# Kernel optimization log

Measured on AMD Instinct MI355X. Metric: run time of the kernel, lower is better.

## Reference

```python
import jax, jax.numpy as jnp
import numpy as np

EMBED = 768
HEADS = 12
HEAD_DIM = EMBED // HEADS
B, S = 1, 4096


def setup_inputs() -> dict:
    key = jax.random.key(0)
    ks = jax.random.split(key, 8)
    values = jax.random.normal(ks[0], (B, S, EMBED), dtype=jnp.float32)
    keys_in = jax.random.normal(ks[1], (B, S, EMBED), dtype=jnp.float32)
    queries = jax.random.normal(ks[2], (B, S, EMBED), dtype=jnp.float32)
    # causal mask: 1.0 where attention is disallowed (gets * -1e9)
    mask = jnp.triu(jnp.ones((S, S), dtype=jnp.float32), k=1)[None, None, :, :]
    sc = 1.0 / np.sqrt(EMBED)
    W_q = jax.random.normal(ks[3], (EMBED, EMBED), dtype=jnp.float32) * sc
    W_k = jax.random.normal(ks[4], (EMBED, EMBED), dtype=jnp.float32) * sc
    W_v = jax.random.normal(ks[5], (EMBED, EMBED), dtype=jnp.float32) * sc
    W_o = jax.random.normal(ks[6], (EMBED, EMBED), dtype=jnp.float32) * sc
    b_o = jnp.zeros((EMBED,), dtype=jnp.float32)
    return {"values": values, "keys": keys_in, "queries": queries, "mask": mask,
            "W_q": W_q, "W_k": W_k, "W_v": W_v, "W_o": W_o, "b_o": b_o}


def reference(values, keys, queries, mask, W_q, W_k, W_v, W_o, b_o):
    N, S_, _ = queries.shape
    # linear projections (Dense, no bias)
    q = queries @ W_q  # [N, S, E]
    k = keys @ W_k
    v = values @ W_v
    # split heads -> [N, H, S, Dh]
    def split(x):
        return x.reshape(N, S_, HEADS, HEAD_DIM).transpose(0, 2, 1, 3)
    q, k, v = split(q), split(k), split(v)
    scores = jnp.einsum('nhqd,nhkd->nhqk', q, k) / jnp.sqrt(
        jnp.asarray(HEAD_DIM, dtype=q.dtype))
    scores = scores + mask * (-1e9)
    attn = jax.nn.softmax(scores, axis=-1)
    out = jnp.einsum('nhqk,nhkd->nhqd', attn, v)  # [N, H, S, Dh]
    out = out.transpose(0, 2, 1, 3).reshape(N, S_, EMBED)
    return out @ W_o + b_o
```

## Files before the change

### kernel.cpp

```cpp
#include <hip/hip_runtime.h>

#define S_LEN 4096
#define EMB   768
#define NH    12
#define DH    64

typedef __attribute__((ext_vector_type(8))) short bf16x8;
typedef __attribute__((ext_vector_type(4))) float f32x4;

__device__ __forceinline__ unsigned short f2bf(float f) {
    union { float f; unsigned u; } v; v.f = f;
    unsigned r = v.u + 0x7fffu + ((v.u >> 16) & 1u);
    return (unsigned short)(r >> 16);
}
__device__ __forceinline__ float bf2f(unsigned short u) {
    union { unsigned u; float f; } v; v.u = (unsigned)u << 16; return v.f;
}
__device__ __forceinline__ unsigned pk2(float lo, float hi) {
    unsigned r;
    asm("v_cvt_pk_bf16_f32 %0, %1, %2" : "=v"(r) : "v"(lo), "v"(hi));
    return r;
}
__device__ __forceinline__ float fexp2(float x) {
    float r;
    asm("v_exp_f32 %0, %1" : "=v"(r) : "v"(x));
    return r;
}
__device__ __forceinline__ f32x4 mfma16(bf16x8 a, bf16x8 b, f32x4 c) {
    return __builtin_amdgcn_mfma_f32_16x16x32_bf16(a, b, c, 0, 0, 0);
}
__device__ __forceinline__ void async16(unsigned short* lds, const unsigned short* g) {
    __builtin_amdgcn_global_load_lds(
        (const __attribute__((address_space(1))) unsigned int*)(const void*)g,
        (__attribute__((address_space(3))) unsigned int*)(void*)lds, 16, 0, 0);
}

#define QSCALE 0.180336884f

__global__ __launch_bounds__(256) void prep(const float* __restrict__ Wq, const float* __restrict__ Wk,
                     const float* __restrict__ Wv, const float* __restrict__ Wo,
                     const float* __restrict__ q_in, const float* __restrict__ k_in,
                     const float* __restrict__ v_in,
                     unsigned short* __restrict__ WT, unsigned short* __restrict__ conv) {
    int bx = blockIdx.x, t = threadIdx.x;
    if (bx < 576) {
        __shared__ float tile[64][65];
        int z = bx / 144, rem = bx % 144;
        int k0 = (rem / 12) * 64, n0 = (rem % 12) * 64;
        const float* W = (z == 0) ? Wq : (z == 1) ? Wk : (z == 2) ? Wv : Wo;
        unsigned short* out = WT + (size_t)z * EMB * EMB;
        int row = t >> 2, c = (t & 3) * 16;
        const float4* src = (const float4*)(W + (size_t)(k0 + row) * EMB + n0 + c);
#pragma unroll
        for (int i = 0; i < 4; i++) {
            float4 v = src[i];
            tile[row][c + i * 4 + 0] = v.x; tile[row][c + i * 4 + 1] = v.y;
            tile[row][c + i * 4 + 2] = v.z; tile[row][c + i * 4 + 3] = v.w;
        }
        __syncthreads();
        unsigned short tmp[16] __attribute__((aligned(16)));
#pragma unroll
        for (int i = 0; i < 16; i++) tmp[i] = f2bf(tile[c + i][row]);
        int4* dst = (int4*)(out + (size_t)(n0 + row) * EMB + k0 + c);
        dst[0] = *(int4*)&tmp[0];
        dst[1] = *(int4*)&tmp[8];
    } else {
        size_t e8 = ((size_t)(bx - 576) * 256 + t) * 8;
        int z = (int)(e8 / 3145728);
        size_t off = e8 - (size_t)z * 3145728;
        const float* src = (z == 0) ? q_in : (z == 1) ? k_in : v_in;
        float4 a = *(const float4*)(src + off);
        float4 b = *(const float4*)(src + off + 4);
        unsigned r[4];
        r[0] = pk2(a.x, a.y); r[1] = pk2(a.z, a.w);
        r[2] = pk2(b.x, b.y); r[3] = pk2(b.z, b.w);
        *(int4*)(conv + e8) = *(int4*)r;
    }
}


__global__ __launch_bounds__(256) void gemm_qkv(const unsigned short* __restrict__ conv,
                                                const unsigned short* __restrict__ WT,
                                                unsigned short* __restrict__ Qh,
                                                unsigned short* __restrict__ Kh,
                                                unsigned short* __restrict__ Vt) {
    __shared__ unsigned short As[128 * 32];
    __shared__ unsigned short Bs[128 * 32];
    int m0 = blockIdx.x * 128;
    int z = blockIdx.y / 6, n0 = (blockIdx.y % 6) * 128;
    const unsigned short* A  = conv + (size_t)z * 3145728;
    const unsigned short* Bt = WT   + (size_t)z * 589824;
    int t = threadIdx.x, lane = t & 63, wv = t >> 6, quad = lane >> 4, l16 = lane & 15;
    int wm = wv >> 1, wn = wv & 1;
    int cfr = (quad ^ ((l16 >> 1) & 3)) * 8;

    const unsigned short* pa[2];
    const unsigned short* pb[2];
#pragma unroll
    for (int a2 = 0; a2 < 2; a2++) {
        int s1 = a2 * 256 + t, r = s1 >> 2, gc = (s1 & 3) ^ ((r >> 1) & 3);
        pa[a2] = A  + (size_t)(m0 + r) * EMB + gc * 8;
        pb[a2] = Bt + (size_t)(n0 + r) * EMB + gc * 8;
    }
    f32x4 acc[4][4] = {};

    for (int k0 = 0; k0 < EMB; k0 += 32) {
#pragma unroll
        for (int a2 = 0; a2 < 2; a2++) {
            async16(&As[(a2 * 256 + t) * 8], pa[a2] + k0);
            async16(&Bs[(a2 * 256 + t) * 8], pb[a2] + k0);
        }
        __syncthreads();
        bf16x8 fa[4], fb[4];
#pragma unroll
        for (int mi = 0; mi < 4; mi++)
            fa[mi] = *(bf16x8*)&As[(wm * 64 + mi * 16 + l16) * 32 + cfr];
#pragma unroll
        for (int ni = 0; ni < 4; ni++)
            fb[ni] = *(bf16x8*)&Bs[(wn * 64 + ni * 16 + l16) * 32 + cfr];
#pragma unroll
        for (int mi = 0; mi < 4; mi++)
#pragma unroll
            for (int ni = 0; ni < 4; ni++)
                acc[mi][ni] = mfma16(fa[mi], fb[ni], acc[mi][ni]);
        __syncthreads();
    }

    if (z == 2) {
#pragma unroll
        for (int mi = 0; mi < 4; mi++)
#pragma unroll
            for (int ni = 0; ni < 4; ni++) {
                int m = m0 + wm * 64 + mi * 16 + quad * 4;
                int n = n0 + wn * 64 + ni * 16 + l16;
                uint2 val;
                val.x = pk2(acc[mi][ni][0], acc[mi][ni][1]);
                val.y = pk2(acc[mi][ni][2], acc[mi][ni][3]);
                *(uint2*)&Vt[(size_t)(((n >> 6) << 6) + (n & 63)) * S_LEN + m] = val;
            }
    } else {
        unsigned short* dst = z ? Kh : Qh;
        float sc = z ? 1.0f : QSCALE;
#pragma unroll
        for (int mi = 0; mi < 4; mi++)
#pragma unroll
            for (int ni = 0; ni < 4; ni++)
#pragma unroll
                for (int r = 0; r < 4; r++) {
                    int m = m0 + wm * 64 + mi * 16 + quad * 4 + r;
                    int n = n0 + wn * 64 + ni * 16 + l16;
                    dst[((size_t)(n >> 6) * S_LEN + m) * 64 + (n & 63)] = f2bf(acc[mi][ni][r] * sc);
                }
    }
}

__global__ __launch_bounds__(256) void attn_kernel(const unsigned short* __restrict__ Qh,
                                                   const unsigned short* __restrict__ Kh,
                                                   const unsigned short* __restrict__ Vt,
                                                   unsigned short* __restrict__ Opart,
                                                   float* __restrict__ Lpart) {
    __shared__ unsigned short Kls[2][4096];
    __shared__ unsigned short Vls[2][4096];
    __shared__ unsigned short Pls[4 * 64 * 72];

    int p = blockIdx.x, h = blockIdx.y;
    int qb = 0, pre = 0, np = 1;
    for (;;) { np = (4 * qb + 9) / 6; if (pre + np > p) break; pre += np; qb++; }
    int sp = p - pre;
    int ntile = 4 * qb + 4;
    int base = ntile / np, rem = ntile % np;
    int jb = sp * base + min(sp, rem);
    int je = jb + base + (sp < rem ? 1 : 0);
    int part = h * 96 + p;
    int q0 = qb << 8;

    int t = threadIdx.x, w = t >> 6, lane = t & 63, quad = lane >> 4, l16 = lane & 15;
    int rb = w * 64;
    int cfr0 = (quad ^ (l16 & 7)) * 8, cfr1 = ((quad + 4) ^ (l16 & 7)) * 8;

    const unsigned short* kb_ = Kh + (size_t)h * S_LEN * DH;
    const unsigned short* vb_ = Vt + (size_t)h * S_LEN * DH;

    bf16x8 aQ[4][2];
#pragma unroll
    for (int rg = 0; rg < 4; rg++)
#pragma unroll
        for (int kh = 0; kh < 2; kh++)
            aQ[rg][kh] = *(const bf16x8*)(Qh + ((size_t)h * S_LEN + q0 + rb + rg * 16 + l16) * 64 + kh * 32 + quad * 8);

    const unsigned short* pk_[2];
    const unsigned short* pv_[2];
#pragma unroll
    for (int a2 = 0; a2 < 2; a2++) {
        int s1 = a2 * 256 + t, r = s1 >> 3, gc = (s1 & 7) ^ (r & 7);
        pk_[a2] = kb_ + (size_t)(jb * 64 + r) * 64 + gc * 8;
        pv_[a2] = vb_ + (size_t)r * S_LEN + jb * 64 + gc * 8;
    }

    f32x4 o[4][4] = {};
    float lsum[4][4] = {};
    unsigned short* pwave = &Pls[w * 64 * 72];

    for (int jt = jb; jt < je; jt++) {
        int buf = (jt - jb) & 1;
        if (jt == jb) {
#pragma unroll
            for (int a2 = 0; a2 < 2; a2++) {
                async16(&Kls[0][(a2 * 256 + t) * 8], pk_[a2]); pk_[a2] += 4096;
                async16(&Vls[0][(a2 * 256 + t) * 8], pv_[a2]); pv_[a2] += 64;
            }
        }
        __syncthreads();
        if (jt + 1 < je) {
#pragma unroll
            for (int a2 = 0; a2 < 2; a2++) {
                async16(&Kls[buf ^ 1][(a2 * 256 + t) * 8], pk_[a2]); pk_[a2] += 4096;
                async16(&Vls[buf ^ 1][(a2 * 256 + t) * 8], pv_[a2]); pv_[a2] += 64;
            }
        }
        int diag = jt - 4 * qb;
        bool active = !(diag >= 0 && w < diag);
        if (active) {
            bf16x8 kf[4][2];
#pragma unroll
            for (int nt = 0; nt < 4; nt++) {
                int row = nt * 16 + l16;
                kf[nt][0] = *(bf16x8*)&Kls[buf][row * 64 + cfr0];
                kf[nt][1] = *(bf16x8*)&Kls[buf][row * 64 + cfr1];
            }
#pragma unroll
            for (int rg = 0; rg < 4; rg++) {
                f32x4 s[4];
#pragma unroll
                for (int nt = 0; nt < 4; nt++) {
                    f32x4 zz = {};
                    zz = mfma16(aQ[rg][0], kf[nt][0], zz);
                    zz = mfma16(aQ[rg][1], kf[nt][1], zz);
                    s[nt] = zz;
                }
                if (diag >= 0) {
                    int dlt = diag * 64;
#pragma unroll
                    for (int nt = 0; nt < 4; nt++) {
                        int col = nt * 16 + l16;
#pragma unroll
                        for (int r = 0; r < 4; r++) {
                            int rel = rb + rg * 16 + quad * 4 + r - dlt;
                            if (col > rel) s[nt][r] = -1e9f;
                        }
                    }
                }
#pragma unroll
                for (int nt = 0; nt < 4; nt++) {
                    float p0 = fexp2(s[nt][0]);
                    float p1 = fexp2(s[nt][1]);
                    float p2 = fexp2(s[nt][2]);
                    float p3 = fexp2(s[nt][3]);
                    lsum[rg][0] += p0; lsum[rg][1] += p1;
                    lsum[rg][2] += p2; lsum[rg][3] += p3;
                    unsigned pa2 = pk2(p0, p1), pb2 = pk2(p2, p3);
                    unsigned short* pw = &pwave[(rg * 16 + quad * 4) * 72 + nt * 16 + l16];
                    pw[0]   = (unsigned short)pa2;
                    pw[72]  = (unsigned short)(pa2 >> 16);
                    pw[144] = (unsigned short)pb2;
                    pw[216] = (unsigned short)(pb2 >> 16);
                }
            }
            asm volatile("s_waitcnt lgkmcnt(0)" ::: "memory");
            bf16x8 bP[4][2];
#pragma unroll
            for (int ntq = 0; ntq < 4; ntq++) {
                bP[ntq][0] = *(bf16x8*)&pwave[(ntq * 16 + l16) * 72 + quad * 8];
                bP[ntq][1] = *(bf16x8*)&pwave[(ntq * 16 + l16) * 72 + 32 + quad * 8];
            }
#pragma unroll
            for (int mt = 0; mt < 4; mt++) {
                int row = mt * 16 + l16;
                bf16x8 v0f = *(bf16x8*)&Vls[buf][row * 64 + cfr0];
                bf16x8 v1f = *(bf16x8*)&Vls[buf][row * 64 + cfr1];
#pragma unroll
                for (int ntq = 0; ntq < 4; ntq++) {
                    o[mt][ntq] = mfma16(v0f, bP[ntq][0], o[mt][ntq]);
                    o[mt][ntq] = mfma16(v1f, bP[ntq][1], o[mt][ntq]);
                }
            }
        }
    }

    unsigned short* op = Opart + (size_t)part * 16384;
#pragma unroll
    for (int mt = 0; mt < 4; mt++)
#pragma unroll
        for (int ntq = 0; ntq < 4; ntq++) {
            uint2 val;
            val.x = pk2(o[mt][ntq][0], o[mt][ntq][1]);
            val.y = pk2(o[mt][ntq][2], o[mt][ntq][3]);
            int q = rb + ntq * 16 + l16;
            int d = mt * 16 + quad * 4;
            *(uint2*)&op[q * 64 + d] = val;
        }
    float* lp = Lpart + (size_t)part * 256;
#pragma unroll
    for (int rg = 0; rg < 4; rg++)
#pragma unroll
        for (int r = 0; r < 4; r++) {
            float v = lsum[rg][r];
            v += __shfl_xor(v, 8); v += __shfl_xor(v, 4);
            v += __shfl_xor(v, 2); v += __shfl_xor(v, 1);
            if (l16 == 0) lp[rb + rg * 16 + quad * 4 + r] = v;
        }
}

__global__ __launch_bounds__(256) void merge(const unsigned short* __restrict__ Opart,
                                             const float* __restrict__ Lpart,
                                             unsigned short* __restrict__ O) {
    int mb = blockIdx.x, h = blockIdx.y;
    int qb = mb >> 1, half = mb & 1;
    int pre = 0;
    for (int q = 0; q < qb; q++) pre += (4 * q + 9) / 6;
    int np = (4 * qb + 9) / 6;
    int pbase = h * 96 + pre;
    int t = threadIdx.x;
    int rloc = half * 128 + (t >> 1), ch = (t & 1) * 32;

    float acc[32] = {};
    float ls = 0.f;
    const unsigned short* src = Opart + (size_t)pbase * 16384 + rloc * 64 + ch;
    for (int p2 = 0; p2 < np; p2++) {
        ls += Lpart[(size_t)(pbase + p2) * 256 + rloc];
        const int4* s4 = (const int4*)(src + (size_t)p2 * 16384);
#pragma unroll
        for (int i = 0; i < 4; i++) {
            int4 x = s4[i];
            const unsigned short* xs = (const unsigned short*)&x;
#pragma unroll
            for (int j = 0; j < 8; j++) acc[i * 8 + j] += bf2f(xs[j]);
        }
    }
    float inv = 1.0f / ls;
    unsigned outp[16];
#pragma unroll
    for (int i = 0; i < 16; i++) outp[i] = pk2(acc[2 * i] * inv, acc[2 * i + 1] * inv);
    int4* dst = (int4*)(O + (size_t)(qb * 256 + rloc) * EMB + h * 64 + ch);
#pragma unroll
    for (int i = 0; i < 4; i++) dst[i] = *(int4*)&outp[i * 4];
}

__global__ __launch_bounds__(256) void gemm_out(const unsigned short* __restrict__ O,
                                                const unsigned short* __restrict__ WT,
                                                const float* __restrict__ bias,
                                                float* __restrict__ out) {
    __shared__ unsigned short As[128 * 32];
    __shared__ unsigned short Bs[64 * 32];
    int m0 = blockIdx.x * 128, n0 = blockIdx.y * 64;
    const unsigned short* Bt = WT + (size_t)3 * 589824;
    int t = threadIdx.x, lane = t & 63, wv = t >> 6, quad = lane >> 4, l16 = lane & 15;
    int wm = wv >> 1, wn = wv & 1;
    int cfr = (quad ^ ((l16 >> 1) & 3)) * 8;

    const unsigned short* pa[2];
    const unsigned short* pb;
#pragma unroll
    for (int a2 = 0; a2 < 2; a2++) {
        int s1 = a2 * 256 + t, r = s1 >> 2, gc = (s1 & 3) ^ ((r >> 1) & 3);
        pa[a2] = O + (size_t)(m0 + r) * EMB + gc * 8;
    }
    {
        int r = t >> 2, gc = (t & 3) ^ ((r >> 1) & 3);
        pb = Bt + (size_t)(n0 + r) * EMB + gc * 8;
    }
    f32x4 acc[4][2] = {};

    for (int k0 = 0; k0 < EMB; k0 += 32) {
#pragma unroll
        for (int a2 = 0; a2 < 2; a2++)
            async16(&As[(a2 * 256 + t) * 8], pa[a2] + k0);
        async16(&Bs[t * 8], pb + k0);
        __syncthreads();
        bf16x8 fa[4], fb[2];
#pragma unroll
        for (int mi = 0; mi < 4; mi++)
            fa[mi] = *(bf16x8*)&As[(wm * 64 + mi * 16 + l16) * 32 + cfr];
#pragma unroll
        for (int ni = 0; ni < 2; ni++)
            fb[ni] = *(bf16x8*)&Bs[(wn * 32 + ni * 16 + l16) * 32 + cfr];
#pragma unroll
        for (int mi = 0; mi < 4; mi++)
#pragma unroll
            for (int ni = 0; ni < 2; ni++)
                acc[mi][ni] = mfma16(fa[mi], fb[ni], acc[mi][ni]);
        __syncthreads();
    }

    float bv[2];
#pragma unroll
    for (int ni = 0; ni < 2; ni++) bv[ni] = bias[n0 + wn * 32 + ni * 16 + l16];
#pragma unroll
    for (int mi = 0; mi < 4; mi++)
#pragma unroll
        for (int ni = 0; ni < 2; ni++)
#pragma unroll
            for (int r = 0; r < 4; r++) {
                int m = m0 + wm * 64 + mi * 16 + quad * 4 + r;
                int n = n0 + wn * 32 + ni * 16 + l16;
                out[(size_t)m * EMB + n] = acc[mi][ni][r] + bv[ni];
            }
}

extern "C" void kernel_launch(void* const* d_in, const int* in_sizes, int n_in,
                              void* d_out, int out_size, void* d_ws, size_t ws_size,
                              hipStream_t stream) {
    const float* values  = (const float*)d_in[0];
    const float* keys    = (const float*)d_in[1];
    const float* queries = (const float*)d_in[2];
    const float* Wq = (const float*)d_in[4];
    const float* Wk = (const float*)d_in[5];
    const float* Wv = (const float*)d_in[6];
    const float* Wo = (const float*)d_in[7];
    const float* bo = (const float*)d_in[8];

    char* ws = (char*)d_ws;
    unsigned short* WT = (unsigned short*)ws;
    unsigned short* Qh = (unsigned short*)(ws + 4718592);
    unsigned short* Kh = (unsigned short*)(ws + 11010048);
    unsigned short* Vt = (unsigned short*)(ws + 17301504);
    unsigned short* O  = (unsigned short*)(ws + 23592960);
    unsigned short* conv = (unsigned short*)(ws + 29884416);
    unsigned short* Op   = (unsigned short*)(ws + 29884416);
    float*          Lp   = (float*)(ws + 29884416 + 37748736);
    float* out = (float*)d_out;

    prep<<<dim3(5184), 256, 0, stream>>>(Wq, Wk, Wv, Wo, queries, keys, values, WT, conv);
    gemm_qkv<<<dim3(32, 18), 256, 0, stream>>>(conv, WT, Qh, Kh, Vt);
    attn_kernel<<<dim3(96, 12), 256, 0, stream>>>(Qh, Kh, Vt, Op, Lp);
    merge<<<dim3(32, 12), 256, 0, stream>>>(Op, Lp, O);
    gemm_out<<<dim3(32, 12), 256, 0, stream>>>(O, WT, bo, out);
}
```

Measured before the change: 292.3 us.

## Shrink attention query block to 128 rows and split keys into fixed 8-tile chunks

The attention kernel now handles 128 query rows per block, 32 per wave, instead of 256. It splits the causal key range into fixed chunks of 8 tiles, which gives 144 partitions per head in place of 96, and the merge kernel's partition indexing is changed to match. The aim is better load balance and more blocks in flight across the CUs, with fewer registers and less LDS per block. In exchange, K/V tiles are reused by fewer query rows, so global and LDS traffic per FLOP rises, and more partial outputs have to be merged.

```diff
diff --git a/kernel.cpp b/kernel.cpp
--- a/kernel.cpp
+++ b/kernel.cpp
@@ -78,7 +78,6 @@
     }
 }
 
-
 __global__ __launch_bounds__(256) void gemm_qkv(const unsigned short* __restrict__ conv,
                                                 const unsigned short* __restrict__ WT,
                                                 unsigned short* __restrict__ Qh,
@@ -161,101 +160,102 @@
                                                    float* __restrict__ Lpart) {
     __shared__ unsigned short Kls[2][4096];
     __shared__ unsigned short Vls[2][4096];
-    __shared__ unsigned short Pls[4 * 64 * 72];
+    __shared__ unsigned short Pls[4 * 32 * 72];
 
     int p = blockIdx.x, h = blockIdx.y;
-    int qb = 0, pre = 0, np = 1;
-    for (;;) { np = (4 * qb + 9) / 6; if (pre + np > p) break; pre += np; qb++; }
+    int qb2 = 0, pre = 0;
+    while (pre + (qb2 >> 2) + 1 <= p) { pre += (qb2 >> 2) + 1; qb2++; }
     int sp = p - pre;
-    int ntile = 4 * qb + 4;
-    int base = ntile / np, rem = ntile % np;
-    int jb = sp * base + min(sp, rem);
-    int je = jb + base + (sp < rem ? 1 : 0);
-    int part = h * 96 + p;
-    int q0 = qb << 8;
+    int part = h * 144 + p;
+    int ntile = 2 * qb2 + 2;
+    int jb = sp * 8, je = min(jb + 8, ntile);
+    int q0 = qb2 << 7;
 
     int t = threadIdx.x, w = t >> 6, lane = t & 63, quad = lane >> 4, l16 = lane & 15;
-    int rb = w * 64;
-    int cfr0 = (quad ^ (l16 & 7)) * 8, cfr1 = ((quad + 4) ^ (l16 & 7)) * 8;
+    int rb = w * 32;
+    int c0 = (quad ^ (l16 & 7)) * 8, c1 = (((quad + 4) ^ (l16 & 7))) * 8;
 
     const unsigned short* kb_ = Kh + (size_t)h * S_LEN * DH;
     const unsigned short* vb_ = Vt + (size_t)h * S_LEN * DH;
 
-    bf16x8 aQ[4][2];
-#pragma unroll
-    for (int rg = 0; rg < 4; rg++)
+    bf16x8 aQ[2][2];
+#pragma unroll
+    for (int rg = 0; rg < 2; rg++)
 #pragma unroll
         for (int kh = 0; kh < 2; kh++)
             aQ[rg][kh] = *(const bf16x8*)(Qh + ((size_t)h * S_LEN + q0 + rb + rg * 16 + l16) * 64 + kh * 32 + quad * 8);
 
     const unsigned short* pk_[2];
     const unsigned short* pv_[2];
+    int ldso[2];
 #pragma unroll
     for (int a2 = 0; a2 < 2; a2++) {
         int s1 = a2 * 256 + t, r = s1 >> 3, gc = (s1 & 7) ^ (r & 7);
         pk_[a2] = kb_ + (size_t)(jb * 64 + r) * 64 + gc * 8;
         pv_[a2] = vb_ + (size_t)r * S_LEN + jb * 64 + gc * 8;
-    }
-
-    f32x4 o[4][4] = {};
-    float lsum[4][4] = {};
-    unsigned short* pwave = &Pls[w * 64 * 72];
-
+        ldso[a2] = s1 * 8;
+    }
+
+    f32x4 o[4][2] = {};
+    float lsum[2][4] = {};
+    unsigned short* pwave = &Pls[w * 32 * 72];
+
+#pragma unroll 1
     for (int jt = jb; jt < je; jt++) {
         int buf = (jt - jb) & 1;
         if (jt == jb) {
 #pragma unroll
             for (int a2 = 0; a2 < 2; a2++) {
-                async16(&Kls[0][(a2 * 256 + t) * 8], pk_[a2]); pk_[a2] += 4096;
-                async16(&Vls[0][(a2 * 256 + t) * 8], pv_[a2]); pv_[a2] += 64;
+                async16(&Kls[0][ldso[a2]], pk_[a2]); pk_[a2] += 4096;
+                async16(&Vls[0][ldso[a2]], pv_[a2]); pv_[a2] += 64;
             }
         }
         __syncthreads();
         if (jt + 1 < je) {
 #pragma unroll
             for (int a2 = 0; a2 < 2; a2++) {
-                async16(&Kls[buf ^ 1][(a2 * 256 + t) * 8], pk_[a2]); pk_[a2] += 4096;
-                async16(&Vls[buf ^ 1][(a2 * 256 + t) * 8], pv_[a2]); pv_[a2] += 64;
-            }
-        }
-        int diag = jt - 4 * qb;
-        bool active = !(diag >= 0 && w < diag);
+                async16(&Kls[buf ^ 1][ldso[a2]], pk_[a2]); pk_[a2] += 4096;
+                async16(&Vls[buf ^ 1][ldso[a2]], pv_[a2]); pv_[a2] += 64;
+            }
+        }
+        bool active = !(jt == 2 * qb2 + 1 && w < 2);
         if (active) {
-            bf16x8 kf[4][2];
+            f32x4 s[2][4];
 #pragma unroll
             for (int nt = 0; nt < 4; nt++) {
                 int row = nt * 16 + l16;
-                kf[nt][0] = *(bf16x8*)&Kls[buf][row * 64 + cfr0];
-                kf[nt][1] = *(bf16x8*)&Kls[buf][row * 64 + cfr1];
-            }
-#pragma unroll
-            for (int rg = 0; rg < 4; rg++) {
-                f32x4 s[4];
-#pragma unroll
-                for (int nt = 0; nt < 4; nt++) {
+                bf16x8 k0f = *(bf16x8*)&Kls[buf][row * 64 + c0];
+                bf16x8 k1f = *(bf16x8*)&Kls[buf][row * 64 + c1];
+#pragma unroll
+                for (int rg = 0; rg < 2; rg++) {
                     f32x4 zz = {};
-                    zz = mfma16(aQ[rg][0], kf[nt][0], zz);
-                    zz = mfma16(aQ[rg][1], kf[nt][1], zz);
-                    s[nt] = zz;
+                    zz = mfma16(aQ[rg][0], k0f, zz);
+                    zz = mfma16(aQ[rg][1], k1f, zz);
+                    s[rg][nt] = zz;
                 }
-                if (diag >= 0) {
-                    int dlt = diag * 64;
+            }
+            if (jt >= 2 * qb2) {
+                int dlt = (jt - 2 * qb2) * 64;
+#pragma unroll
+                for (int rg = 0; rg < 2; rg++)
 #pragma unroll
                     for (int nt = 0; nt < 4; nt++) {
                         int col = nt * 16 + l16;
 #pragma unroll
                         for (int r = 0; r < 4; r++) {
                             int rel = rb + rg * 16 + quad * 4 + r - dlt;
-                            if (col > rel) s[nt][r] = -1e9f;
+                            if (col > rel) s[rg][nt][r] = -1e9f;
                         }
                     }
-                }
+            }
+#pragma unroll
+            for (int rg = 0; rg < 2; rg++)
 #pragma unroll
                 for (int nt = 0; nt < 4; nt++) {
-                    float p0 = fexp2(s[nt][0]);
-                    float p1 = fexp2(s[nt][1]);
-                    float p2 = fexp2(s[nt][2]);
-                    float p3 = fexp2(s[nt][3]);
+                    float p0 = fexp2(s[rg][nt][0]);
+                    float p1 = fexp2(s[rg][nt][1]);
+                    float p2 = fexp2(s[rg][nt][2]);
+                    float p3 = fexp2(s[rg][nt][3]);
                     lsum[rg][0] += p0; lsum[rg][1] += p1;
                     lsum[rg][2] += p2; lsum[rg][3] += p3;
                     unsigned pa2 = pk2(p0, p1), pb2 = pk2(p2, p3);
@@ -265,21 +265,20 @@
                     pw[144] = (unsigned short)pb2;
                     pw[216] = (unsigned short)(pb2 >> 16);
                 }
-            }
             asm volatile("s_waitcnt lgkmcnt(0)" ::: "memory");
-            bf16x8 bP[4][2];
-#pragma unroll
-            for (int ntq = 0; ntq < 4; ntq++) {
+            bf16x8 bP[2][2];
+#pragma unroll
+            for (int ntq = 0; ntq < 2; ntq++) {
                 bP[ntq][0] = *(bf16x8*)&pwave[(ntq * 16 + l16) * 72 + quad * 8];
                 bP[ntq][1] = *(bf16x8*)&pwave[(ntq * 16 + l16) * 72 + 32 + quad * 8];
             }
 #pragma unroll
             for (int mt = 0; mt < 4; mt++) {
                 int row = mt * 16 + l16;
-                bf16x8 v0f = *(bf16x8*)&Vls[buf][row * 64 + cfr0];
-                bf16x8 v1f = *(bf16x8*)&Vls[buf][row * 64 + cfr1];
-#pragma unroll
-                for (int ntq = 0; ntq < 4; ntq++) {
+                bf16x8 v0f = *(bf16x8*)&Vls[buf][row * 64 + c0];
+                bf16x8 v1f = *(bf16x8*)&Vls[buf][row * 64 + c1];
+#pragma unroll
+                for (int ntq = 0; ntq < 2; ntq++) {
                     o[mt][ntq] = mfma16(v0f, bP[ntq][0], o[mt][ntq]);
                     o[mt][ntq] = mfma16(v1f, bP[ntq][1], o[mt][ntq]);
                 }
@@ -287,11 +286,11 @@
         }
     }
 
-    unsigned short* op = Opart + (size_t)part * 16384;
+    unsigned short* op = Opart + (size_t)part * 8192;
 #pragma unroll
     for (int mt = 0; mt < 4; mt++)
 #pragma unroll
-        for (int ntq = 0; ntq < 4; ntq++) {
+        for (int ntq = 0; ntq < 2; ntq++) {
             uint2 val;
             val.x = pk2(o[mt][ntq][0], o[mt][ntq][1]);
             val.y = pk2(o[mt][ntq][2], o[mt][ntq][3]);
@@ -299,9 +298,9 @@
             int d = mt * 16 + quad * 4;
             *(uint2*)&op[q * 64 + d] = val;
         }
-    float* lp = Lpart + (size_t)part * 256;
-#pragma unroll
-    for (int rg = 0; rg < 4; rg++)
+    float* lp = Lpart + (size_t)part * 128;
+#pragma unroll
+    for (int rg = 0; rg < 2; rg++)
 #pragma unroll
         for (int r = 0; r < 4; r++) {
             float v = lsum[rg][r];
@@ -314,21 +313,19 @@
 __global__ __launch_bounds__(256) void merge(const unsigned short* __restrict__ Opart,
                                              const float* __restrict__ Lpart,
                                              unsigned short* __restrict__ O) {
-    int mb = blockIdx.x, h = blockIdx.y;
-    int qb = mb >> 1, half = mb & 1;
-    int pre = 0;
-    for (int q = 0; q < qb; q++) pre += (4 * q + 9) / 6;
-    int np = (4 * qb + 9) / 6;
-    int pbase = h * 96 + pre;
-    int t = threadIdx.x;
-    int rloc = half * 128 + (t >> 1), ch = (t & 1) * 32;
+    int qb2 = blockIdx.x, h = blockIdx.y;
+    int a = qb2 >> 2, b = qb2 & 3;
+    int pre = qb2 + 2 * a * (a - 1) + a * b;
+    int cnt = a + 1;
+    int pbase = h * 144 + pre;
+    int t = threadIdx.x, row = t >> 1, ch = (t & 1) * 32;
 
     float acc[32] = {};
     float ls = 0.f;
-    const unsigned short* src = Opart + (size_t)pbase * 16384 + rloc * 64 + ch;
-    for (int p2 = 0; p2 < np; p2++) {
-        ls += Lpart[(size_t)(pbase + p2) * 256 + rloc];
-        const int4* s4 = (const int4*)(src + (size_t)p2 * 16384);
+    const unsigned short* src = Opart + (size_t)pbase * 8192 + row * 64 + ch;
+    for (int p2 = 0; p2 < cnt; p2++) {
+        ls += Lpart[(size_t)(pbase + p2) * 128 + row];
+        const int4* s4 = (const int4*)(src + (size_t)p2 * 8192);
 #pragma unroll
         for (int i = 0; i < 4; i++) {
             int4 x = s4[i];
@@ -341,7 +338,7 @@
     unsigned outp[16];
 #pragma unroll
     for (int i = 0; i < 16; i++) outp[i] = pk2(acc[2 * i] * inv, acc[2 * i + 1] * inv);
-    int4* dst = (int4*)(O + (size_t)(qb * 256 + rloc) * EMB + h * 64 + ch);
+    int4* dst = (int4*)(O + (size_t)(qb2 * 128 + row) * EMB + h * 64 + ch);
 #pragma unroll
     for (int i = 0; i < 4; i++) dst[i] = *(int4*)&outp[i * 4];
 }
@@ -427,12 +424,12 @@
     unsigned short* O  = (unsigned short*)(ws + 23592960);
     unsigned short* conv = (unsigned short*)(ws + 29884416);
     unsigned short* Op   = (unsigned short*)(ws + 29884416);
-    float*          Lp   = (float*)(ws + 29884416 + 37748736);
+    float*          Lp   = (float*)(ws + 29884416 + 28311552);
     float* out = (float*)d_out;
 
     prep<<<dim3(5184), 256, 0, stream>>>(Wq, Wk, Wv, Wo, queries, keys, values, WT, conv);
     gemm_qkv<<<dim3(32, 18), 256, 0, stream>>>(conv, WT, Qh, Kh, Vt);
-    attn_kernel<<<dim3(96, 12), 256, 0, stream>>>(Qh, Kh, Vt, Op, Lp);
+    attn_kernel<<<dim3(144, 12), 256, 0, stream>>>(Qh, Kh, Vt, Op, Lp);
     merge<<<dim3(32, 12), 256, 0, stream>>>(Op, Lp, O);
     gemm_out<<<dim3(32, 12), 256, 0, stream>>>(O, WT, bo, out);
 }
```

New measurement: 252.4 us. 13.6% less time.
